# Kernel tuning notes

Measured on AMD Instinct MI355X. Metric: run time of the kernel, lower is better.

Reference implementation:

```python
import jax, jax.numpy as jnp
import numpy as np

B, T, C, H = 8, 2048, 1024, 64  # batch, seq (block_size), n_embd, head_size


def setup_inputs() -> dict:
    key = jax.random.key(0)
    kx, kq, kk, kv = jax.random.split(key, 4)
    s = 1.0 / np.sqrt(C)
    return {
        "x": jax.random.normal(kx, (B, T, C), dtype=jnp.float32),
        "Wq": jax.random.normal(kq, (C, H), dtype=jnp.float32) * s,
        "Wk": jax.random.normal(kk, (C, H), dtype=jnp.float32) * s,
        "Wv": jax.random.normal(kv, (C, H), dtype=jnp.float32) * s,
    }


def reference(x, Wq, Wk, Wv):
    t = x.shape[1]
    q = jnp.einsum("btc,ch->bth", x, Wq)
    k = jnp.einsum("btc,ch->bth", x, Wk)
    v = jnp.einsum("btc,ch->bth", x, Wv)
    scores = jnp.einsum("bqh,bkh->bqk", q, k) / jnp.sqrt(jnp.float32(H))
    causal = jnp.tril(jnp.ones((t, t), dtype=bool))  # tril mask
    scores = jnp.where(causal, scores, -jnp.inf)
    attn = jax.nn.softmax(scores, axis=-1)
    return jnp.einsum("bqk,bkh->bqh", attn, v)
```

## Files before the change

kernel.cpp:

```cpp
#include <hip/hip_runtime.h>
#include <hip/hip_bf16.h>

#define BB 8
#define TT 2048
#define CC 1024
#define HH 64

typedef __attribute__((ext_vector_type(8)))  short bf16x8;
typedef __attribute__((ext_vector_type(4)))  float f32x4;
typedef __attribute__((ext_vector_type(16))) float f32x16;
typedef __attribute__((ext_vector_type(8)))  unsigned short us8;
typedef unsigned int u32;

static __device__ __forceinline__ unsigned short f2bf(float f) {
    union { float f; unsigned int u; } v; v.f = f;
    unsigned int u = v.u;
    return (unsigned short)((u + 0x7FFFu + ((u >> 16) & 1u)) >> 16);
}

__global__ __launch_bounds__(256) void prep_weights(
        const float* __restrict__ Wq, const float* __restrict__ Wk,
        const float* __restrict__ Wv, unsigned short* __restrict__ Wt) {
    __shared__ float tile[64][65];
    int w  = blockIdx.x >> 4;
    int c0 = (blockIdx.x & 15) * 64;
    const float* W = (w == 0) ? Wq : (w == 1) ? Wk : Wv;
    int li = threadIdx.x;
    {
        int c = li >> 2, h4 = (li & 3) * 16;
        const float* src = W + (size_t)(c0 + c) * HH + h4;
        #pragma unroll
        for (int i = 0; i < 4; ++i) {
            float4 v4 = *(const float4*)(src + i * 4);
            tile[c][h4 + i*4 + 0] = v4.x; tile[c][h4 + i*4 + 1] = v4.y;
            tile[c][h4 + i*4 + 2] = v4.z; tile[c][h4 + i*4 + 3] = v4.w;
        }
    }
    __syncthreads();
    float scale = (w == 0) ? 0.1803368802f : 1.0f;
    int h = li >> 2, cg = (li & 3) * 16;
    unsigned short* dst = Wt + (size_t)w * HH * CC + (size_t)h * CC + c0 + cg;
    #pragma unroll
    for (int i = 0; i < 16; ++i) dst[i] = f2bf(tile[cg + i][h] * scale);
}

__global__ __launch_bounds__(512, 4) void proj_qkv(
        const float* __restrict__ x, const unsigned short* __restrict__ Wt,
        unsigned short* __restrict__ qws, unsigned short* __restrict__ kws,
        unsigned short* __restrict__ vws) {
    __shared__ unsigned short Xs[2][32 * 64];
    __shared__ unsigned short Ws[2][192 * 64];
    int tid = threadIdx.x;
    int wv = tid >> 6, lane = tid & 63;
    int quad = (lane >> 4) & 3, lq = lane & 15;
    int mg = wv >> 2, ng = wv & 3;
    int r0 = blockIdx.x * 32;

    bool xact = tid < 256;
    int xr = tid >> 3, xg = tid & 7;
    const float* xsrc = x + (size_t)(r0 + xr) * CC + xg * 8;
    int xdst = xr * 64 + ((xg ^ (xr & 7)) * 8);
    float4 xa[2], xb[2];

    f32x4 acc[3];
    #pragma unroll
    for (int nt = 0; nt < 3; ++nt)
        #pragma unroll
        for (int i = 0; i < 4; ++i) acc[nt][i] = 0.0f;

    auto stageW = [&](int buf, int kc) {
        #pragma unroll
        for (int i = 0; i < 3; ++i) {
            int fp = tid + i * 512;
            int r = fp >> 3, pb = fp & 7, g = pb ^ (r & 7);
            const u32 __attribute__((address_space(1)))* gsrc =
                (const u32 __attribute__((address_space(1)))*)
                    (Wt + (size_t)r * CC + kc * 64 + g * 8);
            u32 __attribute__((address_space(3)))* ldst =
                (u32 __attribute__((address_space(3)))*)(&Ws[buf][fp * 8]);
            __builtin_amdgcn_global_load_lds(gsrc, ldst, 16, 0, 0);
        }
    };
    auto loadX = [&](int set, int kc) {
        xa[set] = *(const float4*)(xsrc + kc * 64);
        xb[set] = *(const float4*)(xsrc + kc * 64 + 4);
    };
    auto writeX = [&](int set, int buf) {
        unsigned short h[8];
        h[0]=f2bf(xa[set].x); h[1]=f2bf(xa[set].y);
        h[2]=f2bf(xa[set].z); h[3]=f2bf(xa[set].w);
        h[4]=f2bf(xb[set].x); h[5]=f2bf(xb[set].y);
        h[6]=f2bf(xb[set].z); h[7]=f2bf(xb[set].w);
        *(us8*)&Xs[buf][xdst] = *(const us8*)h;
    };

    if (xact) { loadX(0, 0); loadX(1, 1); }
    stageW(0, 0);
    if (xact) writeX(0, 0);

    for (int kc = 0; kc < 16; ++kc) {
        int cur = kc & 1;
        __syncthreads();
        if (kc < 15) stageW(1 - cur, kc + 1);
        if (xact && kc < 14) loadX(kc & 1, kc + 2);
        #pragma unroll
        for (int ks = 0; ks < 2; ++ks) {
            int g = ks * 4 + quad;
            int arow = mg * 16 + lq;
            bf16x8 a = *(const bf16x8*)&Xs[cur][arow * 64 + (g ^ (lq & 7)) * 8];
            bf16x8 b[3];
            #pragma unroll
            for (int nt = 0; nt < 3; ++nt) {
                int brow = ng * 48 + nt * 16 + lq;
                b[nt] = *(const bf16x8*)&Ws[cur][brow * 64 + (g ^ (lq & 7)) * 8];
            }
            #pragma unroll
            for (int nt = 0; nt < 3; ++nt)
                acc[nt] = __builtin_amdgcn_mfma_f32_16x16x32_bf16(
                    a, b[nt], acc[nt], 0, 0, 0);
        }
        if (xact && kc < 15) writeX((kc + 1) & 1, 1 - cur);
    }

    __syncthreads();
    unsigned short* Vl = (unsigned short*)Xs;
    #pragma unroll
    for (int nt = 0; nt < 3; ++nt) {
        int g = ng * 48 + nt * 16 + lq;
        #pragma unroll
        for (int i = 0; i < 4; ++i) {
            int row = mg * 16 + quad * 4 + i;
            unsigned short bv = f2bf(acc[nt][i]);
            if (g < 64)       qws[(size_t)(r0 + row) * HH + g] = bv;
            else if (g < 128) kws[(size_t)(r0 + row) * HH + (g - 64)] = bv;
            else              Vl[(g - 128) * 36 + row] = bv;
        }
    }
    __syncthreads();
    if (tid < 256) {
        int h = tid >> 2, tb = (tid & 3) * 8;
        int b = r0 >> 11, rr = r0 & (TT - 1);
        *(us8*)(vws + ((size_t)b * HH + h) * TT + rr + tb) =
            *(const us8*)&Vl[h * 36 + tb];
    }
}

__global__ __launch_bounds__(128, 3) void attn(
        const unsigned short* __restrict__ qws,
        const unsigned short* __restrict__ kws,
        const unsigned short* __restrict__ vws,
        float* __restrict__ Op, float* __restrict__ Lp) {
    __shared__ unsigned short Kt[32][72];
    __shared__ unsigned short Vt[64][40];
    __shared__ unsigned short Ps[64][40];
    int ti = blockIdx.x;
    int s  = blockIdx.y;
    int b  = blockIdx.z;
    int last = 2 * ti + 1;
    if (s > last) return;
    int tid = threadIdx.x, wv = tid >> 6, lane = tid & 63;
    int half = lane >> 5, l31 = lane & 31;

    bf16x8 qf[4];
    {
        const unsigned short* qp =
            qws + ((size_t)b * TT + ti * 64 + wv * 32 + l31) * HH + half * 8;
        #pragma unroll
        for (int ks = 0; ks < 4; ++ks) qf[ks] = *(const bf16x8*)(qp + ks * 16);
    }
    f32x16 O0, O1, Lc;
    #pragma unroll
    for (int i = 0; i < 16; ++i) { O0[i] = 0.f; O1[i] = 0.f; Lc[i] = 0.f; }
    bf16x8 ones;
    #pragma unroll
    for (int i = 0; i < 8; ++i) ones[i] = (short)0x3F80;

    for (int jc = s; jc <= last; jc += 4) {
        __syncthreads();
        #pragma unroll
        for (int i = 0; i < 2; ++i) {
            int slot = tid + i * 128;
            int r = slot >> 3, g = slot & 7;
            *(us8*)&Kt[r][g * 8] =
                *(const us8*)(kws + ((size_t)b * TT + jc * 32 + r) * HH + g * 8);
        }
        #pragma unroll
        for (int i = 0; i < 2; ++i) {
            int slot = tid + i * 128;
            int h = slot >> 2, kb = slot & 3;
            *(us8*)&Vt[h][kb * 8] =
                *(const us8*)(vws + ((size_t)b * HH + h) * TT + jc * 32 + kb * 8);
        }
        __syncthreads();
        f32x16 S;
        #pragma unroll
        for (int i = 0; i < 16; ++i) S[i] = 0.f;
        #pragma unroll
        for (int ks = 0; ks < 4; ++ks) {
            bf16x8 kf = *(const bf16x8*)&Kt[l31][ks * 16 + half * 8];
            S = __builtin_amdgcn_mfma_f32_32x32x16_bf16(qf[ks], kf, S, 0, 0, 0);
        }
        bool diag = (jc >= 2 * ti + wv);
        #pragma unroll
        for (int r = 0; r < 16; ++r) {
            int pat = (r & 3) + 8 * (r >> 2) + 4 * half;
            float p = __builtin_amdgcn_exp2f(S[r]);
            if (diag && jc * 32 + l31 > ti * 64 + wv * 32 + pat) p = 0.0f;
            Ps[wv * 32 + pat][l31] = f2bf(p);
        }
        #pragma unroll
        for (int ks = 0; ks < 2; ++ks) {
            bf16x8 pa  = *(const bf16x8*)&Ps[wv * 32 + l31][ks * 16 + half * 8];
            bf16x8 vf0 = *(const bf16x8*)&Vt[l31][ks * 16 + half * 8];
            bf16x8 vf1 = *(const bf16x8*)&Vt[32 + l31][ks * 16 + half * 8];
            O0 = __builtin_amdgcn_mfma_f32_32x32x16_bf16(pa, vf0, O0, 0, 0, 0);
            O1 = __builtin_amdgcn_mfma_f32_32x32x16_bf16(pa, vf1, O1, 0, 0, 0);
            Lc = __builtin_amdgcn_mfma_f32_32x32x16_bf16(pa, ones, Lc, 0, 0, 0);
        }
    }
    float* Ob = Op + (((size_t)s * BB + b) * TT + ti * 64 + wv * 32) * HH;
    #pragma unroll
    for (int r = 0; r < 16; ++r) {
        int pat = (r & 3) + 8 * (r >> 2) + 4 * half;
        Ob[(size_t)pat * HH + l31]      = O0[r];
        Ob[(size_t)pat * HH + 32 + l31] = O1[r];
    }
    if (l31 == 0) {
        #pragma unroll
        for (int r = 0; r < 16; ++r) {
            int pat = (r & 3) + 8 * (r >> 2) + 4 * half;
            Lp[((size_t)s * BB + b) * TT + ti * 64 + wv * 32 + pat] = Lc[r];
        }
    }
}

__global__ __launch_bounds__(256) void norm_out(
        const float* __restrict__ Op, const float* __restrict__ Lp,
        float* __restrict__ out) {
    int idx = blockIdx.x * 256 + threadIdx.x;
    int g = idx >> 4;
    int ti = (g & (TT - 1)) >> 6;
    int ns = min(2 * ti + 2, 4);
    float4 a = make_float4(0.f, 0.f, 0.f, 0.f);
    float Ls = 0.f;
    for (int s = 0; s < ns; ++s) {
        float4 v = ((const float4*)(Op + ((size_t)s * BB * TT + g) * HH))[idx & 15];
        a.x += v.x; a.y += v.y; a.z += v.z; a.w += v.w;
        Ls += Lp[(size_t)s * BB * TT + g];
    }
    float inv = 1.0f / Ls;
    a.x *= inv; a.y *= inv; a.z *= inv; a.w *= inv;
    ((float4*)out)[idx] = a;
}

extern "C" void kernel_launch(void* const* d_in, const int* in_sizes, int n_in,
                              void* d_out, int out_size, void* d_ws, size_t ws_size,
                              hipStream_t stream) {
    (void)in_sizes; (void)n_in; (void)out_size; (void)ws_size;
    const float* x  = (const float*)d_in[0];
    const float* Wq = (const float*)d_in[1];
    const float* Wk = (const float*)d_in[2];
    const float* Wv = (const float*)d_in[3];
    float* out = (float*)d_out;

    char* ws = (char*)d_ws;
    unsigned short* Wt  = (unsigned short*)ws;
    unsigned short* qws = (unsigned short*)(ws + (1u << 19));
    unsigned short* kws = (unsigned short*)(ws + (1u << 19) + (1u << 21));
    unsigned short* vws = (unsigned short*)(ws + (1u << 19) + (2u << 21));
    float*          Op  = (float*)(ws + (1u << 19) + (3u << 21));
    float*          Lp  = (float*)(ws + (1u << 19) + (3u << 21) + (1u << 24));

    prep_weights<<<48, 256, 0, stream>>>(Wq, Wk, Wv, Wt);
    proj_qkv<<<512, 512, 0, stream>>>(x, Wt, qws, kws, vws);
    attn<<<dim3(32, 4, 8), 128, 0, stream>>>(qws, kws, vws, Op, Lp);
    norm_out<<<1024, 256, 0, stream>>>(Op, Lp, out);
}
```

Baseline: 138.2 us.

## Double the KV split count and store attention partials in bf16

Result: no change. 139.6 us (+1.0%).

```diff
diff --git a/kernel.cpp b/kernel.cpp
--- a/kernel.cpp
+++ b/kernel.cpp
@@ -5,6 +5,7 @@
 #define TT 2048
 #define CC 1024
 #define HH 64
+#define NSPLIT 8
 
 typedef __attribute__((ext_vector_type(8)))  short bf16x8;
 typedef __attribute__((ext_vector_type(4)))  float f32x4;
@@ -16,6 +17,9 @@
     union { float f; unsigned int u; } v; v.f = f;
     unsigned int u = v.u;
     return (unsigned short)((u + 0x7FFFu + ((u >> 16) & 1u)) >> 16);
+}
+static __device__ __forceinline__ float bf2f(unsigned short s) {
+    union { u32 u; float f; } v; v.u = ((u32)s) << 16; return v.f;
 }
 
 __global__ __launch_bounds__(256) void prep_weights(
@@ -149,7 +153,7 @@
         const unsigned short* __restrict__ qws,
         const unsigned short* __restrict__ kws,
         const unsigned short* __restrict__ vws,
-        float* __restrict__ Op, float* __restrict__ Lp) {
+        unsigned short* __restrict__ Op, float* __restrict__ Lp) {
     __shared__ unsigned short Kt[32][72];
     __shared__ unsigned short Vt[64][40];
     __shared__ unsigned short Ps[64][40];
@@ -175,7 +179,7 @@
     #pragma unroll
     for (int i = 0; i < 8; ++i) ones[i] = (short)0x3F80;
 
-    for (int jc = s; jc <= last; jc += 4) {
+    for (int jc = s; jc <= last; jc += NSPLIT) {
         __syncthreads();
         #pragma unroll
         for (int i = 0; i < 2; ++i) {
@@ -218,12 +222,13 @@
             Lc = __builtin_amdgcn_mfma_f32_32x32x16_bf16(pa, ones, Lc, 0, 0, 0);
         }
     }
-    float* Ob = Op + (((size_t)s * BB + b) * TT + ti * 64 + wv * 32) * HH;
+    unsigned short* Ob =
+        Op + (((size_t)s * BB + b) * TT + ti * 64 + wv * 32) * HH;
     #pragma unroll
     for (int r = 0; r < 16; ++r) {
         int pat = (r & 3) + 8 * (r >> 2) + 4 * half;
-        Ob[(size_t)pat * HH + l31]      = O0[r];
-        Ob[(size_t)pat * HH + 32 + l31] = O1[r];
+        Ob[(size_t)pat * HH + l31]      = f2bf(O0[r]);
+        Ob[(size_t)pat * HH + 32 + l31] = f2bf(O1[r]);
     }
     if (l31 == 0) {
         #pragma unroll
@@ -235,22 +240,34 @@
 }
 
 __global__ __launch_bounds__(256) void norm_out(
-        const float* __restrict__ Op, const float* __restrict__ Lp,
+        const unsigned short* __restrict__ Op, const float* __restrict__ Lp,
         float* __restrict__ out) {
     int idx = blockIdx.x * 256 + threadIdx.x;
-    int g = idx >> 4;
+    int g = idx >> 2;
+    int hseg = (idx & 3) * 16;
     int ti = (g & (TT - 1)) >> 6;
-    int ns = min(2 * ti + 2, 4);
-    float4 a = make_float4(0.f, 0.f, 0.f, 0.f);
+    int ns = min(2 * ti + 2, NSPLIT);
+    float a[16];
+    #pragma unroll
+    for (int j = 0; j < 16; ++j) a[j] = 0.f;
     float Ls = 0.f;
     for (int s = 0; s < ns; ++s) {
-        float4 v = ((const float4*)(Op + ((size_t)s * BB * TT + g) * HH))[idx & 15];
-        a.x += v.x; a.y += v.y; a.z += v.z; a.w += v.w;
+        const unsigned short* base =
+            Op + ((size_t)s * BB * TT + g) * HH + hseg;
+        us8 u0 = *(const us8*)base;
+        us8 u1 = *(const us8*)(base + 8);
+        #pragma unroll
+        for (int j = 0; j < 8; ++j) { a[j] += bf2f(u0[j]); a[8 + j] += bf2f(u1[j]); }
         Ls += Lp[(size_t)s * BB * TT + g];
     }
     float inv = 1.0f / Ls;
-    a.x *= inv; a.y *= inv; a.z *= inv; a.w *= inv;
-    ((float4*)out)[idx] = a;
+    float* ob = out + (size_t)g * HH + hseg;
+    #pragma unroll
+    for (int q = 0; q < 4; ++q) {
+        float4 v = make_float4(a[q*4] * inv, a[q*4+1] * inv,
+                               a[q*4+2] * inv, a[q*4+3] * inv);
+        ((float4*)ob)[q] = v;
+    }
 }
 
 extern "C" void kernel_launch(void* const* d_in, const int* in_sizes, int n_in,
@@ -268,11 +285,11 @@
     unsigned short* qws = (unsigned short*)(ws + (1u << 19));
     unsigned short* kws = (unsigned short*)(ws + (1u << 19) + (1u << 21));
     unsigned short* vws = (unsigned short*)(ws + (1u << 19) + (2u << 21));
-    float*          Op  = (float*)(ws + (1u << 19) + (3u << 21));
+    unsigned short* Op  = (unsigned short*)(ws + (1u << 19) + (3u << 21));
     float*          Lp  = (float*)(ws + (1u << 19) + (3u << 21) + (1u << 24));
 
     prep_weights<<<48, 256, 0, stream>>>(Wq, Wk, Wv, Wt);
     proj_qkv<<<512, 512, 0, stream>>>(x, Wt, qws, kws, vws);
-    attn<<<dim3(32, 4, 8), 128, 0, stream>>>(qws, kws, vws, Op, Lp);
-    norm_out<<<1024, 256, 0, stream>>>(Op, Lp, out);
-}
+    attn<<<dim3(32, NSPLIT, 8), 128, 0, stream>>>(qws, kws, vws, Op, Lp);
+    norm_out<<<256, 256, 0, stream>>>(Op, Lp, out);
+}
```
